# Kernel tuning notes

Hardware: AMD Instinct MI355X
Metric: run time of the kernel (lower is better)

## Reference

```python
import jax, jax.numpy as jnp
import numpy as np

B, N_CAM, J = 8, 5, 15        # batch, cameras, joints
H, W = 128, 240               # heatmap h, w  (HEATMAP_SIZE = [240, 128] = [w, h])
VX, VY, VZ = 80, 80, 20       # voxels_per_axis
NBINS = VX * VY * VZ          # 128000


def setup_inputs() -> dict:
    key = jax.random.key(0)
    k1, k2 = jax.random.split(key)
    heatmaps = jax.random.uniform(k1, (B, N_CAM, J, H, W), dtype=jnp.float32)
    # cached projected sampling grid, clamped to [-1.1, 1.1] as in project_grid
    sample_grid = jax.random.uniform(k2, (N_CAM, NBINS, 2), dtype=jnp.float32,
                                     minval=-1.1, maxval=1.1)
    return {"heatmaps": heatmaps, "sample_grid": sample_grid}


def _grid_sample_bilinear(hm, grid):
    """F.grid_sample(mode='bilinear', padding_mode='zeros', align_corners=True).

    hm:   [B, n, J, H, W]
    grid: [n, nbins, 2]  normalized (x, y) in roughly [-1.1, 1.1]
    returns [B, n, J, nbins]
    """
    Bv, n, Jv, Hv, Wv = hm.shape
    nb = grid.shape[1]
    gx, gy = grid[..., 0], grid[..., 1]
    # align_corners=True mapping from [-1, 1] to pixel coords
    ix = (gx + 1.0) * 0.5 * (Wv - 1)
    iy = (gy + 1.0) * 0.5 * (Hv - 1)
    x0 = jnp.floor(ix)
    y0 = jnp.floor(iy)
    x1 = x0 + 1.0
    y1 = y0 + 1.0
    wx1 = ix - x0
    wx0 = 1.0 - wx1
    wy1 = iy - y0
    wy0 = 1.0 - wy1

    hmf = hm.reshape(Bv, n, Jv, Hv * Wv)

    def gather(yi, xi):
        # zeros padding: out-of-range corners contribute 0
        valid = ((xi >= 0) & (xi <= Wv - 1) & (yi >= 0) & (yi <= Hv - 1))
        xc = jnp.clip(xi, 0, Wv - 1).astype(jnp.int32)
        yc = jnp.clip(yi, 0, Hv - 1).astype(jnp.int32)
        idx = yc * Wv + xc                                   # [n, nb]
        idxb = jnp.broadcast_to(idx[None, :, None, :], (Bv, n, Jv, nb))
        vals = jnp.take_along_axis(hmf, idxb, axis=3)        # [B, n, J, nb]
        return vals * valid[None, :, None, :].astype(hm.dtype)

    out = (gather(y0, x0) * (wy0 * wx0)[None, :, None, :]
           + gather(y0, x1) * (wy0 * wx1)[None, :, None, :]
           + gather(y1, x0) * (wy1 * wx0)[None, :, None, :]
           + gather(y1, x1) * (wy1 * wx1)[None, :, None, :])
    return out


def reference(heatmaps, sample_grid):
    sampled = _grid_sample_bilinear(heatmaps, sample_grid)   # [B, n, J, nbins]
    cubes = jnp.clip(jnp.mean(sampled, axis=1), 0.0, 1.0)    # mean over cameras
    return cubes.reshape(heatmaps.shape[0], heatmaps.shape[2], VX, VY, VZ)
```

## Files before the change

### kernel.cpp

```cpp
#include <hip/hip_runtime.h>
#include <hip/hip_fp16.h>

#define B_     8
#define NCAM   5
#define J_     15
#define H_     128
#define W_     240
#define NB     128000
#define HW_    (H_ * W_)
#define PAIR_ROWS (H_ / 2)
#define PAIR_DW  (PAIR_ROWS * W_)
#define SMEM_BYTES (PAIR_DW * 4)
#define PAIR_G4  (PAIR_DW / 4)
#define TPB    1024
#define NCHUNK 8
#define BPB    (NB / NCHUNK)
#define ITEMS  16
#define NBJ    (B_ * J_)
#define NBLK   (NBJ * NCHUNK)

typedef __fp16 fp16x2 __attribute__((ext_vector_type(2)));

__device__ __forceinline__ unsigned int pkrtz(float lo, float hi) {
    fp16x2 h = __builtin_amdgcn_cvt_pkrtz(lo, hi);
    return __builtin_bit_cast(unsigned int, h);
}

__device__ __forceinline__ void bilinear_rec(float gx, float gy,
                                             unsigned int& addr,
                                             unsigned int& w0pk,
                                             unsigned int& w1pk) {
    const float ix = (gx + 1.0f) * (0.5f * (W_ - 1));
    const float iy = (gy + 1.0f) * (0.5f * (H_ - 1));
    const float x0f = floorf(ix);
    const float y0f = floorf(iy);
    const float wx1 = ix - x0f, wx0 = 1.0f - wx1;
    const float wy1 = iy - y0f, wy0 = 1.0f - wy1;
    const int x0 = (int)x0f;
    const int y0 = (int)y0f;
    const int xc = min(max(x0, 0), W_ - 2);
    const int yc = min(max(y0, 0), H_ - 2);
    const float vx0 = (x0 >= 0  && x0 <= W_ - 1) ? wx0 : 0.0f;
    const float vx1 = (x0 >= -1 && x0 <= W_ - 2) ? wx1 : 0.0f;
    const float vy0 = (y0 >= 0  && y0 <= H_ - 1) ? wy0 : 0.0f;
    const float vy1 = (y0 >= -1 && y0 <= H_ - 2) ? wy1 : 0.0f;
    const bool xhi = (x0 == W_ - 1);
    const bool xlo = (x0 == -1);
    const bool yhi = (y0 == H_ - 1);
    const bool ylo = (y0 == -1);
    const float a0 = (xhi ? 0.0f : vx0) + (xlo ? vx1 : 0.0f);
    const float a1 = (xhi ? vx0 : 0.0f) + (xlo ? 0.0f : vx1);
    const float b0 = (yhi ? 0.0f : vy0) + (ylo ? vy1 : 0.0f);
    const float b1 = (yhi ? vy0 : 0.0f) + (ylo ? 0.0f : vy1);
    const int yp  = yc >> 1;
    const int odd = yc & 1;
    addr = (unsigned int)(yp * W_ + xc) | ((unsigned int)odd << 14);
    w0pk = pkrtz(0.2f * (a0 * b0), 0.2f * (a0 * b1));
    w1pk = pkrtz(0.2f * (a1 * b0), 0.2f * (a1 * b1));
}

__global__ __launch_bounds__(256) void weights_kernel(
    const float* __restrict__ sgrid,
    unsigned short* __restrict__ addr16,
    uint2* __restrict__ wpk)
{
    const int i = blockIdx.x * 256 + threadIdx.x;
    if (i >= NCAM * NB) return;
    const float2 g = ((const float2*)sgrid)[i];
    unsigned int a, w0, w1;
    bilinear_rec(g.x, g.y, a, w0, w1);
    addr16[i] = (unsigned short)a;
    wpk[i] = make_uint2(w0, w1);
}

__device__ __forceinline__ void stage_pairs(const float* __restrict__ img,
                                            unsigned int* s_img, int tid) {
    const float4* __restrict__ src4 = (const float4*)img;
    uint4* dst = (uint4*)s_img;
    for (int gi = tid; gi < PAIR_G4; gi += TPB) {
        const int y2 = gi / (W_ / 4);
        const int xg = gi - y2 * (W_ / 4);
        const float4 t  = src4[120 * y2 + xg];
        const float4 bo = src4[120 * y2 + 60 + xg];
        uint4 d;
        d.x = pkrtz(t.x, bo.x);
        d.y = pkrtz(t.y, bo.y);
        d.z = pkrtz(t.z, bo.z);
        d.w = pkrtz(t.w, bo.w);
        dst[gi] = d;
    }
}

__device__ __forceinline__ float sample_pair(const unsigned int* s_img,
                                             unsigned int a16,
                                             unsigned int w0, unsigned int w1) {
    const unsigned int odd = a16 >> 14;
    const unsigned int a   = a16 & 0x3FFFu;
    const unsigned int sel = 0x03020100u + odd * 0x02020202u;
    const unsigned int* base = s_img + a;
    const unsigned int d_a0 = base[0];
    const unsigned int d_a1 = base[1];
    const unsigned int off  = odd * (unsigned int)W_;
    const unsigned int d_b0 = base[off];
    const unsigned int d_b1 = base[off + 1];
    const unsigned int c0 = __builtin_amdgcn_perm(d_b0, d_a0, sel);
    const unsigned int c1 = __builtin_amdgcn_perm(d_b1, d_a1, sel);
    __half2 p = __hmul2(__builtin_bit_cast(__half2, c0),
                        __builtin_bit_cast(__half2, w0));
    p = __hfma2(__builtin_bit_cast(__half2, c1),
                __builtin_bit_cast(__half2, w1), p);
    return __low2float(p) + __high2float(p);
}

__global__ __launch_bounds__(TPB, 8) void project_kernel(
    const float* __restrict__ hm,
    const unsigned short* __restrict__ addr16,
    const uint2* __restrict__ wpk,
    float* __restrict__ out)
{
    extern __shared__ unsigned int s_img[];
    const int tid   = threadIdx.x;
    const int bj    = blockIdx.x % NBJ;
    const int chunk = blockIdx.x / NBJ;
    const int b     = bj / J_;
    const int j     = bj % J_;
    const int bin0  = chunk * BPB;

    float acc[ITEMS];
#pragma unroll
    for (int it = 0; it < ITEMS; ++it) acc[it] = 0.0f;

    for (int n = 0; n < NCAM; ++n) {
        __syncthreads();
        stage_pairs(hm + (((size_t)b * NCAM + n) * J_ + j) * HW_, s_img, tid);
        __syncthreads();
        const unsigned short* __restrict__ ap = addr16 + n * NB + bin0;
        const uint2* __restrict__ wp = wpk + n * NB + bin0;
#pragma unroll
        for (int it = 0; it < ITEMS; ++it) {
            const int r = it * TPB + tid;
            if (r < BPB) {
                acc[it] += sample_pair(s_img, ap[r], wp[r].x, wp[r].y);
            }
        }
    }

    float* __restrict__ o = out + (size_t)bj * NB + bin0;
#pragma unroll
    for (int it = 0; it < ITEMS; ++it) {
        const int r = it * TPB + tid;
        if (r < BPB) o[r] = fminf(fmaxf(acc[it], 0.0f), 1.0f);
    }
}

#define FB_SMEM   (HW_ * 4)
#define FB_NCHUNK 5
#define FB_BPB    (NB / FB_NCHUNK)
#define FB_ITEMS  (FB_BPB / TPB)
__global__ __launch_bounds__(TPB) void project_fallback(
    const float* __restrict__ hm,
    const float* __restrict__ sgrid,
    float* __restrict__ out)
{
    extern __shared__ float s_f32[];
    const int tid   = threadIdx.x;
    const int bj    = blockIdx.x % NBJ;
    const int chunk = blockIdx.x / NBJ;
    const int b     = bj / J_;
    const int j     = bj % J_;
    const int bin0  = chunk * FB_BPB;

    float acc[FB_ITEMS];
#pragma unroll
    for (int it = 0; it < FB_ITEMS; ++it) acc[it] = 0.0f;

    for (int n = 0; n < NCAM; ++n) {
        __syncthreads();
        const float4* __restrict__ src =
            (const float4*)(hm + (((size_t)b * NCAM + n) * J_ + j) * HW_);
        float4* dst = (float4*)s_f32;
        for (int i = tid; i < HW_ / 4; i += TPB) dst[i] = src[i];
        __syncthreads();
        const float2* __restrict__ g2 = (const float2*)sgrid + n * NB + bin0;
#pragma unroll
        for (int it = 0; it < FB_ITEMS; ++it) {
            const float2 g = g2[it * TPB + tid];
            const float ix = (g.x + 1.0f) * (0.5f * (W_ - 1));
            const float iy = (g.y + 1.0f) * (0.5f * (H_ - 1));
            const float x0f = floorf(ix), y0f = floorf(iy);
            const float wx1 = ix - x0f, wx0 = 1.0f - wx1;
            const float wy1 = iy - y0f, wy0 = 1.0f - wy1;
            const int x0 = (int)x0f, y0 = (int)y0f;
            const int xc = min(max(x0, 0), W_ - 2);
            const int yc = min(max(y0, 0), H_ - 2);
            const float vx0 = (x0 >= 0  && x0 <= W_ - 1) ? wx0 : 0.0f;
            const float vx1 = (x0 >= -1 && x0 <= W_ - 2) ? wx1 : 0.0f;
            const float vy0 = (y0 >= 0  && y0 <= H_ - 1) ? wy0 : 0.0f;
            const float vy1 = (y0 >= -1 && y0 <= H_ - 2) ? wy1 : 0.0f;
            const bool xhi = (x0 == W_ - 1), xlo = (x0 == -1);
            const bool yhi = (y0 == H_ - 1), ylo = (y0 == -1);
            const float a0 = (xhi ? 0.0f : vx0) + (xlo ? vx1 : 0.0f);
            const float a1 = (xhi ? vx0 : 0.0f) + (xlo ? 0.0f : vx1);
            const float b0 = (yhi ? 0.0f : vy0) + (ylo ? vy1 : 0.0f);
            const float b1 = (yhi ? vy0 : 0.0f) + (ylo ? 0.0f : vy1);
            const float* r0 = s_f32 + (yc * W_ + xc);
            acc[it] += b0 * (a0 * r0[0] + a1 * r0[1])
                     + b1 * (a0 * r0[W_] + a1 * r0[W_ + 1]);
        }
    }
    float* __restrict__ o = out + (size_t)bj * NB + bin0;
#pragma unroll
    for (int it = 0; it < FB_ITEMS; ++it)
        o[it * TPB + tid] = fminf(fmaxf(acc[it] * 0.2f, 0.0f), 1.0f);
}

extern "C" void kernel_launch(void* const* d_in, const int* in_sizes, int n_in,
                              void* d_out, int out_size, void* d_ws, size_t ws_size,
                              hipStream_t stream) {
    const float* hm = (const float*)d_in[0];
    const float* sg = (const float*)d_in[1];
    float* out = (float*)d_out;

    (void)hipFuncSetAttribute((const void*)project_fallback,
                              hipFuncAttributeMaxDynamicSharedMemorySize, FB_SMEM);

    const size_t addr_bytes = (size_t)NCAM * NB * sizeof(unsigned short);
    const size_t wpk_bytes  = (size_t)NCAM * NB * sizeof(uint2);
    if (ws_size >= addr_bytes + wpk_bytes) {
        unsigned short* addr16 = (unsigned short*)d_ws;
        uint2* wpk = (uint2*)((char*)d_ws + addr_bytes);
        weights_kernel<<<(NCAM * NB + 255) / 256, 256, 0, stream>>>(sg, addr16, wpk);
        project_kernel<<<NBLK, TPB, SMEM_BYTES, stream>>>(hm, addr16, wpk, out);
    } else {
        project_fallback<<<NBJ * FB_NCHUNK, TPB, FB_SMEM, stream>>>(hm, sg, out);
    }
}
```

Before: 225.7 us.

## Stage overlapping row-pair fp16 layout so each sample needs two LDS reads

Each shared-memory word now packs row y and row y+1 as fp16, for all 127 overlapping row pairs. A bilinear sample therefore needs only two 32-bit LDS reads and no byte-permute select, where it previously needed four. Shared memory grows to about 122 KB per block, which cuts occupancy to one 1024-thread block per CU. The per-block work doubles (4 chunks, 32 items) to spread the larger staging cost over more bins, which raises register pressure.

```diff
diff --git a/kernel.cpp b/kernel.cpp
--- a/kernel.cpp
+++ b/kernel.cpp
@@ -8,14 +8,14 @@
 #define W_     240
 #define NB     128000
 #define HW_    (H_ * W_)
-#define PAIR_ROWS (H_ / 2)
-#define PAIR_DW  (PAIR_ROWS * W_)
-#define SMEM_BYTES (PAIR_DW * 4)
-#define PAIR_G4  (PAIR_DW / 4)
+#define OV_ROWS (H_ - 1)
+#define OV_DW   (OV_ROWS * W_)
+#define SMEM_BYTES (OV_DW * 4)
+#define OV_G4   (OV_DW / 4)
 #define TPB    1024
-#define NCHUNK 8
+#define NCHUNK 4
 #define BPB    (NB / NCHUNK)
-#define ITEMS  16
+#define ITEMS  32
 #define NBJ    (B_ * J_)
 #define NBLK   (NBJ * NCHUNK)
 
@@ -52,9 +52,7 @@
     const float a1 = (xhi ? vx0 : 0.0f) + (xlo ? 0.0f : vx1);
     const float b0 = (yhi ? 0.0f : vy0) + (ylo ? vy1 : 0.0f);
     const float b1 = (yhi ? vy0 : 0.0f) + (ylo ? 0.0f : vy1);
-    const int yp  = yc >> 1;
-    const int odd = yc & 1;
-    addr = (unsigned int)(yp * W_ + xc) | ((unsigned int)odd << 14);
+    addr = (unsigned int)(yc * W_ + xc);
     w0pk = pkrtz(0.2f * (a0 * b0), 0.2f * (a0 * b1));
     w1pk = pkrtz(0.2f * (a1 * b0), 0.2f * (a1 * b1));
 }
@@ -73,46 +71,38 @@
     wpk[i] = make_uint2(w0, w1);
 }
 
-__device__ __forceinline__ void stage_pairs(const float* __restrict__ img,
-                                            unsigned int* s_img, int tid) {
+__device__ __forceinline__ void stage_overlap(const float* __restrict__ img,
+                                              unsigned int* s_img, int tid) {
     const float4* __restrict__ src4 = (const float4*)img;
     uint4* dst = (uint4*)s_img;
-    for (int gi = tid; gi < PAIR_G4; gi += TPB) {
-        const int y2 = gi / (W_ / 4);
-        const int xg = gi - y2 * (W_ / 4);
-        const float4 t  = src4[120 * y2 + xg];
-        const float4 bo = src4[120 * y2 + 60 + xg];
+    for (int gi = tid; gi < OV_G4; gi += TPB) {
+        const int y  = gi / 60;
+        const int xg = gi - y * 60;
+        const float4 t = src4[y * 60 + xg];
+        const float4 b = src4[y * 60 + 60 + xg];
         uint4 d;
-        d.x = pkrtz(t.x, bo.x);
-        d.y = pkrtz(t.y, bo.y);
-        d.z = pkrtz(t.z, bo.z);
-        d.w = pkrtz(t.w, bo.w);
+        d.x = pkrtz(t.x, b.x);
+        d.y = pkrtz(t.y, b.y);
+        d.z = pkrtz(t.z, b.z);
+        d.w = pkrtz(t.w, b.w);
         dst[gi] = d;
     }
 }
 
-__device__ __forceinline__ float sample_pair(const unsigned int* s_img,
-                                             unsigned int a16,
-                                             unsigned int w0, unsigned int w1) {
-    const unsigned int odd = a16 >> 14;
-    const unsigned int a   = a16 & 0x3FFFu;
-    const unsigned int sel = 0x03020100u + odd * 0x02020202u;
-    const unsigned int* base = s_img + a;
-    const unsigned int d_a0 = base[0];
-    const unsigned int d_a1 = base[1];
-    const unsigned int off  = odd * (unsigned int)W_;
-    const unsigned int d_b0 = base[off];
-    const unsigned int d_b1 = base[off + 1];
-    const unsigned int c0 = __builtin_amdgcn_perm(d_b0, d_a0, sel);
-    const unsigned int c1 = __builtin_amdgcn_perm(d_b1, d_a1, sel);
-    __half2 p = __hmul2(__builtin_bit_cast(__half2, c0),
+__device__ __forceinline__ float sample_ov(const unsigned int* s_img,
+                                           unsigned int a16,
+                                           unsigned int w0, unsigned int w1) {
+    const unsigned int* base = s_img + a16;
+    const unsigned int d0 = base[0];
+    const unsigned int d1 = base[1];
+    __half2 p = __hmul2(__builtin_bit_cast(__half2, d0),
                         __builtin_bit_cast(__half2, w0));
-    p = __hfma2(__builtin_bit_cast(__half2, c1),
+    p = __hfma2(__builtin_bit_cast(__half2, d1),
                 __builtin_bit_cast(__half2, w1), p);
     return __low2float(p) + __high2float(p);
 }
 
-__global__ __launch_bounds__(TPB, 8) void project_kernel(
+__global__ __launch_bounds__(TPB, 4) void project_kernel(
     const float* __restrict__ hm,
     const unsigned short* __restrict__ addr16,
     const uint2* __restrict__ wpk,
@@ -132,7 +122,7 @@
 
     for (int n = 0; n < NCAM; ++n) {
         __syncthreads();
-        stage_pairs(hm + (((size_t)b * NCAM + n) * J_ + j) * HW_, s_img, tid);
+        stage_overlap(hm + (((size_t)b * NCAM + n) * J_ + j) * HW_, s_img, tid);
         __syncthreads();
         const unsigned short* __restrict__ ap = addr16 + n * NB + bin0;
         const uint2* __restrict__ wp = wpk + n * NB + bin0;
@@ -140,7 +130,7 @@
         for (int it = 0; it < ITEMS; ++it) {
             const int r = it * TPB + tid;
             if (r < BPB) {
-                acc[it] += sample_pair(s_img, ap[r], wp[r].x, wp[r].y);
+                acc[it] += sample_ov(s_img, ap[r], wp[r].x, wp[r].y);
             }
         }
     }
@@ -221,6 +211,8 @@
     const float* sg = (const float*)d_in[1];
     float* out = (float*)d_out;
 
+    (void)hipFuncSetAttribute((const void*)project_kernel,
+                              hipFuncAttributeMaxDynamicSharedMemorySize, SMEM_BYTES);
     (void)hipFuncSetAttribute((const void*)project_fallback,
                               hipFuncAttributeMaxDynamicSharedMemorySize, FB_SMEM);
 
```

New measurement: 213.3 us. -5.5%, faster.
